# Kernel optimization log

Hardware: AMD Instinct MI355X
Metric: run time of the kernel (lower is better)

## Reference

```python
import jax, jax.numpy as jnp
import numpy as np

INPUT_DIM, HIDDEN_DIM, OUTPUT_DIM = 64, 256, 32
BATCH, SEQ = 256, 1024
# AutoNCP(256, 32, sparsity_level=0.5): motor=32, command=max(int(0.4*224),1)=89, inter=135
LAYER_HID = [135, 89, 32]
LAYER_IN = [INPUT_DIM, 135, 89]


def setup_inputs() -> dict:
    key = jax.random.key(0)
    ks = iter(jax.random.split(key, 64))
    d = {}
    d["x"] = jax.random.normal(next(ks), (BATCH, SEQ, INPUT_DIM), dtype=jnp.float32)
    for l, (fin, hid) in enumerate(zip(LAYER_IN, LAYER_HID)):
        sp = jax.random.bernoulli(next(ks), 0.5, (hid, fin))
        d[f"mask{l}"] = jnp.concatenate([sp, jnp.ones((hid, hid), dtype=bool)], axis=1)
        scale = 1.0 / np.sqrt(fin + hid)
        for name in ("W1", "W2", "Wa", "Wb"):
            d[f"{name}_{l}"] = jax.random.normal(next(ks), (hid, fin + hid), dtype=jnp.float32) * scale
        for name in ("b1", "b2", "ba", "bb"):
            d[f"{name}_{l}"] = jnp.zeros((hid,), dtype=jnp.float32)
    d["fc_W"] = jax.random.normal(next(ks), (HIDDEN_DIM, HIDDEN_DIM), dtype=jnp.float32) * (1.0 / np.sqrt(HIDDEN_DIM))
    d["fc_b"] = jnp.zeros((HIDDEN_DIM,), dtype=jnp.float32)
    return d


def _cfc_cell(inp, h, mask, W1, b1, W2, b2, Wa, ba, Wb, bb):
    # ncps CfCCell, mode='default', no backbone, ts = 1.0
    x = jnp.concatenate([inp, h], axis=1)
    m = mask.astype(W1.dtype)
    ff1 = jnp.tanh(x @ (W1 * m).T + b1)
    ff2 = jnp.tanh(x @ (W2 * m).T + b2)
    t = jax.nn.sigmoid(x @ Wa.T + ba + x @ Wb.T + bb)  # sigmoid(t_a*ts + t_b), ts=1
    return ff1 * (1.0 - t) + t * ff2


def _forward(x, masks, layer_params, fc_W, fc_b):
    B = x.shape[0]
    init = tuple(jnp.zeros((B, h), dtype=x.dtype) for h in LAYER_HID)

    def step(carry, xt):
        hs = list(carry)
        inp = xt
        for l in range(3):  # inter -> command -> motor (WiredCfCCell)
            hs[l] = _cfc_cell(inp, hs[l], masks[l], *layer_params[l])
            inp = hs[l]
        return tuple(hs), None

    carry, _ = jax.lax.scan(step, init, jnp.swapaxes(x, 0, 1))  # scan over time [T,B,D]
    hn = jnp.concatenate(carry, axis=1)  # [B, HIDDEN_DIM] full state
    return hn @ fc_W.T + fc_b


def reference(x, mask0, mask1, mask2,
              W1_0, b1_0, W2_0, b2_0, Wa_0, ba_0, Wb_0, bb_0,
              W1_1, b1_1, W2_1, b2_1, Wa_1, ba_1, Wb_1, bb_1,
              W1_2, b1_2, W2_2, b2_2, Wa_2, ba_2, Wb_2, bb_2,
              fc_W, fc_b):
    masks = (mask0, mask1, mask2)
    lp = ((W1_0, b1_0, W2_0, b2_0, Wa_0, ba_0, Wb_0, bb_0),
          (W1_1, b1_1, W2_1, b2_1, Wa_1, ba_1, Wb_1, bb_1),
          (W1_2, b1_2, W2_2, b2_2, Wa_2, ba_2, Wb_2, bb_2))
    return _forward(x, masks, lp, fc_W, fc_b)
```

## Files before the change

kernel.cpp:

```cpp
#include <hip/hip_runtime.h>


typedef _Float16 half2v __attribute__((ext_vector_type(2)));
typedef _Float16 half8v __attribute__((ext_vector_type(8)));

#define NBLK   256
#define NTHR   512
#define TSTEPS 1024
#define KPAD   224
#define KHALF  112
#define NKB    14

struct Ptrs {
    const float* x;
    const unsigned int* msk[3];
    const float* W1[3];
    const float* W2[3];
    const float* Wa[3];
    const float* Wb[3];
    const float* b1[3];
    const float* b2[3];
    const float* ba[3];
    const float* bb[3];
    const float* fcW;
    const float* fcb;
};

__device__ __forceinline__ float fexp2(float x) {
#if __has_builtin(__builtin_amdgcn_exp2f)
    return __builtin_amdgcn_exp2f(x);
#else
    return exp2f(x);
#endif
}
__device__ __forceinline__ float frcp(float x) {
#if __has_builtin(__builtin_amdgcn_rcpf)
    return __builtin_amdgcn_rcpf(x);
#else
    return 1.0f / x;
#endif
}
__device__ __forceinline__ float fsig(float x) {
    return frcp(1.0f + fexp2(-1.442695041f * x));
}
__device__ __forceinline__ float ftanh(float x) {
    return 2.0f * frcp(1.0f + fexp2(-2.885390082f * x)) - 1.0f;
}

#if __has_builtin(__builtin_amdgcn_fdot2)
#define FD(a, b, c) __builtin_amdgcn_fdot2((a), (b), (c), false)
#else
__device__ __forceinline__ float fd_fallback(half2v a, half2v b, float c) {
    return c + (float)a[0] * (float)b[0] + (float)a[1] * (float)b[1];
}
#define FD(a, b, c) fd_fallback((a), (b), (c))
#endif

__global__ __launch_bounds__(NTHR)
__attribute__((amdgpu_waves_per_eu(2, 2)))
void cfc_kernel(Ptrs P, float* __restrict__ out) {
    __shared__ __align__(16) _Float16 xc[2][3][KPAD];
    __shared__ __align__(16) float hn[256];

    const int tid  = threadIdx.x;
    const int b    = blockIdx.x;
    const int pair = tid >> 1;
    const int half = tid & 1;

    int L, n;
    if (pair < 135)      { L = 0; n = pair; }
    else if (pair < 224) { L = 1; n = pair - 135; }
    else                 { L = 2; n = pair - 224; }
    const int K    = (L == 0) ? 199 : ((L == 1) ? 224 : 121);
    const int HOFF = (L == 0) ? 0   : ((L == 1) ? 135 : 224);

    {
        int* z = (int*)&xc[0][0][0];
        for (int i = tid; i < 2 * 3 * KPAD / 2; i += NTHR) z[i] = 0;
    }
    __syncthreads();

    const int xlane = tid - 448;
    float xpend = 0.0f;
    if (xlane >= 0) {
        xc[0][0][xlane] = (_Float16)P.x[((size_t)b * TSTEPS + 0) * 64 + xlane];
        xpend           = P.x[((size_t)b * TSTEPS + 1) * 64 + xlane];
    }

    const float* W1p        = P.W1[L];
    const float* W2p        = P.W2[L];
    const float* Wap        = P.Wa[L];
    const float* Wbp        = P.Wb[L];
    const unsigned int* mkp = P.msk[L];
    const int nK   = n * K;
    const int koff = half * KHALF;

    half2v wr1[KHALF / 2], wr2[KHALF / 2], wra[KHALF / 2];
#pragma unroll
    for (int i = 0; i < KHALF / 2; ++i) {
        const int k0 = koff + 2 * i, k1 = koff + 2 * i + 1;
        float u0 = 0.f, u1 = 0.f, v0 = 0.f, v1 = 0.f, a0 = 0.f, a1 = 0.f;
        if (k0 < K) {
            const int idx = nK + k0;
            const float mm = (mkp[idx] != 0u) ? 1.0f : 0.0f;
            u0 = W1p[idx] * mm;
            v0 = W2p[idx] * mm;
            a0 = Wap[idx] + Wbp[idx];
        }
        if (k1 < K) {
            const int idx = nK + k1;
            const float mm = (mkp[idx] != 0u) ? 1.0f : 0.0f;
            u1 = W1p[idx] * mm;
            v1 = W2p[idx] * mm;
            a1 = Wap[idx] + Wbp[idx];
        }
        wr1[i] = half2v{(_Float16)u0, (_Float16)u1};
        wr2[i] = half2v{(_Float16)v0, (_Float16)v1};
        wra[i] = half2v{(_Float16)a0, (_Float16)a1};
    }
    const float bv1 = P.b1[L][n];
    const float bv2 = P.b2[L][n];
    const float bva = P.ba[L][n] + P.bb[L][n];
    __syncthreads();

    for (int tick = 0; tick < TSTEPS + 2; ++tick) {
        if (xlane >= 0) {
            if (tick + 1 < TSTEPS)
                xc[(tick + 1) & 1][0][xlane] = (_Float16)xpend;
            if (tick + 2 < TSTEPS)
                xpend = P.x[((size_t)b * TSTEPS + (tick + 2)) * 64 + xlane];
        }

        const int s = tick - L;
        if (s >= 0 && s < TSTEPS) {
            const _Float16* src = &xc[s & 1][L][koff];
            float ac00 = 0.f, ac01 = 0.f, ac10 = 0.f, ac11 = 0.f, ac20 = 0.f, ac21 = 0.f;
#pragma unroll
            for (int kb = 0; kb < NKB; ++kb) {
                const half8v xv = *(const half8v*)(src + kb * 8);
                const half2v x0 = {xv[0], xv[1]};
                const half2v x1 = {xv[2], xv[3]};
                const half2v x2 = {xv[4], xv[5]};
                const half2v x3 = {xv[6], xv[7]};
                const int k4 = kb * 4;
                ac00 = FD(x0, wr1[k4 + 0], ac00);
                ac10 = FD(x0, wr2[k4 + 0], ac10);
                ac20 = FD(x0, wra[k4 + 0], ac20);
                ac01 = FD(x1, wr1[k4 + 1], ac01);
                ac11 = FD(x1, wr2[k4 + 1], ac11);
                ac21 = FD(x1, wra[k4 + 1], ac21);
                ac00 = FD(x2, wr1[k4 + 2], ac00);
                ac10 = FD(x2, wr2[k4 + 2], ac10);
                ac20 = FD(x2, wra[k4 + 2], ac20);
                ac01 = FD(x3, wr1[k4 + 3], ac01);
                ac11 = FD(x3, wr2[k4 + 3], ac11);
                ac21 = FD(x3, wra[k4 + 3], ac21);
            }
            float s1 = ac00 + ac01;
            float s2 = ac10 + ac11;
            float sa = ac20 + ac21;
            s1 += __shfl_xor(s1, 1, 64);
            s2 += __shfl_xor(s2, 1, 64);
            sa += __shfl_xor(sa, 1, 64);
            const float f1 = ftanh(s1 + bv1);
            const float f2 = ftanh(s2 + bv2);
            const float tg = fsig(sa + bva);
            const float h  = f1 + tg * (f2 - f1);
            const _Float16 hv = (_Float16)h;

            const int pA = s & 1;
            const int pB = (s + 1) & 1;
            if (half == 0) {
                if (L == 0)      xc[pA][1][n] = hv;
                else if (L == 1) xc[pA][2][n] = hv;
                if (s == TSTEPS - 1) hn[HOFF + n] = h;
            } else {
                if (L == 0)      xc[pB][0][64 + n]  = hv;
                else if (L == 1) xc[pB][1][135 + n] = hv;
                else             xc[pB][2][89 + n]  = hv;
            }
        }
        __syncthreads();
    }

    {
        const int o = pair;
        const float4* wr = (const float4*)(P.fcW + (size_t)o * 256 + half * 128);
        const float4* hr = (const float4*)(hn + half * 128);
        float acc = half ? 0.0f : P.fcb[o];
#pragma unroll 8
        for (int d = 0; d < 32; ++d) {
            const float4 a = hr[d];
            const float4 w = wr[d];
            acc += a.x * w.x + a.y * w.y + a.z * w.z + a.w * w.w;
        }
        acc += __shfl_xor(acc, 1, 64);
        if (half == 0) out[(size_t)b * 256 + o] = acc;
    }
}

extern "C" void kernel_launch(void* const* d_in, const int* in_sizes, int n_in,
                              void* d_out, int out_size, void* d_ws, size_t ws_size,
                              hipStream_t stream) {
    (void)in_sizes; (void)n_in; (void)out_size; (void)d_ws; (void)ws_size;
    Ptrs P;
    P.x = (const float*)d_in[0];
    for (int l = 0; l < 3; ++l) {
        const int base = 1 + l * 9;
        P.msk[l] = (const unsigned int*)d_in[base + 0];
        P.W1[l]  = (const float*)d_in[base + 1];
        P.W2[l]  = (const float*)d_in[base + 2];
        P.Wa[l]  = (const float*)d_in[base + 3];
        P.Wb[l]  = (const float*)d_in[base + 4];
        P.b1[l]  = (const float*)d_in[base + 5];
        P.b2[l]  = (const float*)d_in[base + 6];
        P.ba[l]  = (const float*)d_in[base + 7];
        P.bb[l]  = (const float*)d_in[base + 8];
    }
    P.fcW = (const float*)d_in[28];
    P.fcb = (const float*)d_in[29];

    hipLaunchKernelGGL(cfc_kernel, dim3(NBLK), dim3(NTHR), 0, stream,
                       P, (float*)d_out);
}
```

Before: 1.463 ms.

## Split each neuron's dot product across four lanes with 1024-thread blocks

Each output neuron is now computed by four threads, each covering a quarter of the K dimension (56 elements), instead of two threads covering 112 each. The block size doubles to 1024 threads, and the per-thread weight register arrays are halved. This shortens the serial dot-product chain on the recurrent critical path each timestep, in exchange for an extra cross-lane shuffle reduction stage and more waves synchronising at every barrier. The final FC layer is also split across four lanes.

```diff
diff --git a/kernel.cpp b/kernel.cpp
--- a/kernel.cpp
+++ b/kernel.cpp
@@ -5,11 +5,11 @@
 typedef _Float16 half8v __attribute__((ext_vector_type(8)));
 
 #define NBLK   256
-#define NTHR   512
+#define NTHR   1024
 #define TSTEPS 1024
 #define KPAD   224
-#define KHALF  112
-#define NKB    14
+#define KQ     56
+#define NKB    7
 
 struct Ptrs {
     const float* x;
@@ -57,20 +57,20 @@
 #endif
 
 __global__ __launch_bounds__(NTHR)
-__attribute__((amdgpu_waves_per_eu(2, 2)))
+__attribute__((amdgpu_waves_per_eu(4, 4)))
 void cfc_kernel(Ptrs P, float* __restrict__ out) {
     __shared__ __align__(16) _Float16 xc[2][3][KPAD];
     __shared__ __align__(16) float hn[256];
 
     const int tid  = threadIdx.x;
     const int b    = blockIdx.x;
-    const int pair = tid >> 1;
-    const int half = tid & 1;
+    const int unit = tid >> 2;
+    const int q    = tid & 3;
 
     int L, n;
-    if (pair < 135)      { L = 0; n = pair; }
-    else if (pair < 224) { L = 1; n = pair - 135; }
-    else                 { L = 2; n = pair - 224; }
+    if (unit < 135)      { L = 0; n = unit; }
+    else if (unit < 224) { L = 1; n = unit - 135; }
+    else                 { L = 2; n = unit - 224; }
     const int K    = (L == 0) ? 199 : ((L == 1) ? 224 : 121);
     const int HOFF = (L == 0) ? 0   : ((L == 1) ? 135 : 224);
 
@@ -80,7 +80,7 @@
     }
     __syncthreads();
 
-    const int xlane = tid - 448;
+    const int xlane = tid - 960;
     float xpend = 0.0f;
     if (xlane >= 0) {
         xc[0][0][xlane] = (_Float16)P.x[((size_t)b * TSTEPS + 0) * 64 + xlane];
@@ -93,11 +93,11 @@
     const float* Wbp        = P.Wb[L];
     const unsigned int* mkp = P.msk[L];
     const int nK   = n * K;
-    const int koff = half * KHALF;
-
-    half2v wr1[KHALF / 2], wr2[KHALF / 2], wra[KHALF / 2];
+    const int koff = q * KQ;
+
+    half2v wr1[KQ / 2], wr2[KQ / 2], wra[KQ / 2];
 #pragma unroll
-    for (int i = 0; i < KHALF / 2; ++i) {
+    for (int i = 0; i < KQ / 2; ++i) {
         const int k0 = koff + 2 * i, k1 = koff + 2 * i + 1;
         float u0 = 0.f, u1 = 0.f, v0 = 0.f, v1 = 0.f, a0 = 0.f, a1 = 0.f;
         if (k0 < K) {
@@ -134,7 +134,7 @@
         const int s = tick - L;
         if (s >= 0 && s < TSTEPS) {
             const _Float16* src = &xc[s & 1][L][koff];
-            float ac00 = 0.f, ac01 = 0.f, ac10 = 0.f, ac11 = 0.f, ac20 = 0.f, ac21 = 0.f;
+            float ac0 = 0.f, ac1 = 0.f, ac2 = 0.f, ac3 = 0.f, ac4 = 0.f, ac5 = 0.f;
 #pragma unroll
             for (int kb = 0; kb < NKB; ++kb) {
                 const half8v xv = *(const half8v*)(src + kb * 8);
@@ -143,25 +143,28 @@
                 const half2v x2 = {xv[4], xv[5]};
                 const half2v x3 = {xv[6], xv[7]};
                 const int k4 = kb * 4;
-                ac00 = FD(x0, wr1[k4 + 0], ac00);
-                ac10 = FD(x0, wr2[k4 + 0], ac10);
-                ac20 = FD(x0, wra[k4 + 0], ac20);
-                ac01 = FD(x1, wr1[k4 + 1], ac01);
-                ac11 = FD(x1, wr2[k4 + 1], ac11);
-                ac21 = FD(x1, wra[k4 + 1], ac21);
-                ac00 = FD(x2, wr1[k4 + 2], ac00);
-                ac10 = FD(x2, wr2[k4 + 2], ac10);
-                ac20 = FD(x2, wra[k4 + 2], ac20);
-                ac01 = FD(x3, wr1[k4 + 3], ac01);
-                ac11 = FD(x3, wr2[k4 + 3], ac11);
-                ac21 = FD(x3, wra[k4 + 3], ac21);
+                ac0 = FD(x0, wr1[k4 + 0], ac0);
+                ac2 = FD(x0, wr2[k4 + 0], ac2);
+                ac4 = FD(x0, wra[k4 + 0], ac4);
+                ac1 = FD(x1, wr1[k4 + 1], ac1);
+                ac3 = FD(x1, wr2[k4 + 1], ac3);
+                ac5 = FD(x1, wra[k4 + 1], ac5);
+                ac0 = FD(x2, wr1[k4 + 2], ac0);
+                ac2 = FD(x2, wr2[k4 + 2], ac2);
+                ac4 = FD(x2, wra[k4 + 2], ac4);
+                ac1 = FD(x3, wr1[k4 + 3], ac1);
+                ac3 = FD(x3, wr2[k4 + 3], ac3);
+                ac5 = FD(x3, wra[k4 + 3], ac5);
             }
-            float s1 = ac00 + ac01;
-            float s2 = ac10 + ac11;
-            float sa = ac20 + ac21;
+            float s1 = ac0 + ac1;
+            float s2 = ac2 + ac3;
+            float sa = ac4 + ac5;
             s1 += __shfl_xor(s1, 1, 64);
             s2 += __shfl_xor(s2, 1, 64);
             sa += __shfl_xor(sa, 1, 64);
+            s1 += __shfl_xor(s1, 2, 64);
+            s2 += __shfl_xor(s2, 2, 64);
+            sa += __shfl_xor(sa, 2, 64);
             const float f1 = ftanh(s1 + bv1);
             const float f2 = ftanh(s2 + bv2);
             const float tg = fsig(sa + bva);
@@ -170,11 +173,11 @@
 
             const int pA = s & 1;
             const int pB = (s + 1) & 1;
-            if (half == 0) {
+            if (q == 0) {
                 if (L == 0)      xc[pA][1][n] = hv;
                 else if (L == 1) xc[pA][2][n] = hv;
                 if (s == TSTEPS - 1) hn[HOFF + n] = h;
-            } else {
+            } else if (q == 1) {
                 if (L == 0)      xc[pB][0][64 + n]  = hv;
                 else if (L == 1) xc[pB][1][135 + n] = hv;
                 else             xc[pB][2][89 + n]  = hv;
@@ -184,18 +187,19 @@
     }
 
     {
-        const int o = pair;
-        const float4* wr = (const float4*)(P.fcW + (size_t)o * 256 + half * 128);
-        const float4* hr = (const float4*)(hn + half * 128);
-        float acc = half ? 0.0f : P.fcb[o];
-#pragma unroll 8
-        for (int d = 0; d < 32; ++d) {
+        const int o = unit;
+        const float4* wr = (const float4*)(P.fcW + (size_t)o * 256 + q * 64);
+        const float4* hr = (const float4*)(hn + q * 64);
+        float acc = (q == 0) ? P.fcb[o] : 0.0f;
+#pragma unroll
+        for (int d = 0; d < 16; ++d) {
             const float4 a = hr[d];
             const float4 w = wr[d];
             acc += a.x * w.x + a.y * w.y + a.z * w.z + a.w * w.w;
         }
         acc += __shfl_xor(acc, 1, 64);
-        if (half == 0) out[(size_t)b * 256 + o] = acc;
+        acc += __shfl_xor(acc, 2, 64);
+        if (q == 0) out[(size_t)b * 256 + o] = acc;
     }
 }
 
```

After: 1.712 ms. 17.0% more time.
